# Optimization experiments

Measured on AMD Instinct MI355X. Metric: run time of the kernel, lower is better.

The kernel has to match this reference:

```python
import jax, jax.numpy as jnp
import numpy as np
from jax import lax

NI, NH, NO = 128, 64, 128
PERIODS = np.array([1, 2, 4, 8, 16, 32, 64, 128], dtype=np.int32)
NCLOCKS = len(PERIODS)
K = NCLOCKS * NH  # total hidden size = 512
T, B = 512, 256


def _glorotize(W):
    W = W * np.sqrt(6.0)
    W = W / np.sqrt(np.sum(W.shape))
    return W


def _recurrent_mask():
    # block upper-triangular: row block r can read hidden blocks r..NCLOCKS-1
    rows = []
    for c in range(NCLOCKS, 0, -1):
        zero = np.zeros((NH, NH * (NCLOCKS - c)))
        one = np.ones((NH, NH * c))
        rows.append(np.concatenate([zero, one], axis=1))
    return np.concatenate(rows, axis=0)


def setup_inputs() -> dict:
    key = jax.random.key(0)
    kx = jax.random.fold_in(key, 0)
    rng = np.random.default_rng(0)
    X = jax.random.normal(kx, (T, B, NI), dtype=jnp.float32)
    Wi = _glorotize(rng.standard_normal((K, NI + 1)))
    Wh = rng.standard_normal((K, K + 1))
    U, _, _ = np.linalg.svd(Wh[:, :-1])
    Wh[:, :-1] = U * _recurrent_mask()
    Wo = _glorotize(rng.standard_normal((NO, K + 1)))
    return {
        "X": X,
        "Wi": jnp.asarray(Wi, jnp.float32),
        "Wh": jnp.asarray(Wh, jnp.float32),
        "Wo": jnp.asarray(Wo, jnp.float32),
    }


def reference(X, Wi, Wh, Wo):
    # X: (T, B, NI). Original code treats trailing axis as batch after transpose.
    periods = jnp.repeat(jnp.asarray(PERIODS), NH)               # (K,)
    active = ((jnp.arange(T)[:, None] % periods[None, :]) == 0)  # (T, K)
    active = active.astype(X.dtype)

    Xt = jnp.swapaxes(X, 1, 2)                                   # (T, NI, B)
    Wi_w, Wi_b = Wi[:, :-1], Wi[:, -1:]                          # (K,NI),(K,1)
    Wh_w, Wh_b = Wh[:, :-1], Wh[:, -1:]                          # (K,K),(K,1)
    Wo_w, Wo_b = Wo[:, :-1], Wo[:, -1:]                          # (NO,K),(NO,1)

    def step(H_prev, inp):
        x, a = inp                                               # (NI,B),(K,)
        i_h = Wi_w @ x + Wi_b                                    # (K,B)
        H_new = jnp.tanh(i_h + Wh_w @ H_prev + Wh_b)             # (K,B)
        a = a[:, None]
        H = a * H_new + (1.0 - a) * H_prev                       # clock gating
        y = jnp.tanh(Wo_w @ H + Wo_b)                            # (NO,B)
        return H, y

    H0 = jnp.zeros((K, B), dtype=X.dtype)
    H, Ys = lax.scan(step, H0, (Xt, active))                     # Ys: (T,NO,B)
    return jnp.swapaxes(Ys, 1, 2), H                             # (T,B,NO),(K,B)
```

## Files before the change

### kernel.cpp

```cpp
#include <hip/hip_runtime.h>


typedef unsigned int  u32;
typedef unsigned short u16;
typedef _Float16 f16;
typedef f16   f16x2 __attribute__((ext_vector_type(2)));
typedef f16   f16x8 __attribute__((ext_vector_type(8)));
typedef float f32x4 __attribute__((ext_vector_type(4)));

#define TT   512
#define BB   256
#define NI_  128
#define NO_  128

#define WIP_N   32768
#define WHRP_N  49152
#define WHLP_N  30720
#define WOA_N   32768
#define ICOMP_PER_B 65280
#define IOFF(j_) (65536 - (65536 >> (j_)))

__device__ __forceinline__ u32 pk2(float a, float b){
  f16x2 v; v.x=(f16)a; v.y=(f16)b; return __builtin_bit_cast(u32, v);
}
__device__ __forceinline__ float tanh_fast(float x){
  float e = __expf(2.0f*x);
  return 1.0f - 2.0f/(e + 1.0f);
}
__device__ __forceinline__ float dot2(u32 a, u32 b, float c){
#if __has_builtin(__builtin_amdgcn_fdot2)
  return __builtin_amdgcn_fdot2(__builtin_bit_cast(f16x2,a), __builtin_bit_cast(f16x2,b), c, false);
#else
  f16x2 x = __builtin_bit_cast(f16x2,a), y = __builtin_bit_cast(f16x2,b);
  c = fmaf((float)x.x,(float)y.x,c); c = fmaf((float)x.y,(float)y.y,c); return c;
#endif
}
__device__ __forceinline__ float f16at_rt(uint4 v, int i){
  u32 w = (i&4) ? ((i&2)? v.w : v.z) : ((i&2)? v.y : v.x);
  w = (i&1) ? (w>>16) : (w & 0xffffu);
  return (float)__builtin_bit_cast(f16, (u16)w);
}
__device__ __forceinline__ float f16at2(uint2 v, int i){
  u32 w = (i&2) ? v.y : v.x;
  w = (i&1) ? (w>>16) : (w & 0xffffu);
  return (float)__builtin_bit_cast(f16, (u16)w);
}
__device__ __forceinline__ float f16at1(u32 v, int i){
  u32 w = i ? (v>>16) : (v & 0xffffu);
  return (float)__builtin_bit_cast(f16, (u16)w);
}

#define BAR()   asm volatile("s_waitcnt lgkmcnt(0)\n\ts_barrier" ::: "memory")
#define LGKMW() do{ asm volatile("s_waitcnt lgkmcnt(0)" ::: "memory"); \
                    __builtin_amdgcn_sched_barrier(0); }while(0)

__global__ __launch_bounds__(256) void cw_prep(
    const float* __restrict__ Wi, const float* __restrict__ Wh, const float* __restrict__ Wo,
    u32* __restrict__ WiP, u32* __restrict__ WhrP, u32* __restrict__ WhlP, u32* __restrict__ WoAu,
    float* __restrict__ cb, float* __restrict__ wob)
{
  const int NTOT = WIP_N + WHRP_N + WHLP_N + WOA_N + 512 + 128;
  for (int idx = blockIdx.x*blockDim.x + threadIdx.x; idx < NTOT; idx += (int)(gridDim.x*blockDim.x)){
    if (idx < WIP_N){
      int r  = idx >> 6;
      int c2 = idx & 63;
      WiP[idx] = pk2(Wi[r*129 + 2*c2], Wi[r*129 + 2*c2 + 1]);
    } else if (idx < WIP_N + WHRP_N){
      int q32 = idx - WIP_N;
      int slot = q32 >> 11, rr = (q32 >> 5) & 63, c4 = q32 & 31;
      int jj = slot / 3, dq = slot % 3, qq = jj + dq;
      u32 v = 0u;
      if (qq <= 7){
        int row = 64*jj + rr;
        v = pk2(Wh[row*513 + 64*qq + 2*c4], Wh[row*513 + 64*qq + 2*c4 + 1]);
      }
      WhrP[q32] = v;
    } else if (idx < WIP_N + WHRP_N + WHLP_N){
      int q32 = idx - WIP_N - WHRP_N;
      int slot = q32 >> 11, rr = (q32 >> 5) & 63, pos = (q32 >> 2) & 7, e = q32 & 3;
      int jj, qq;
      if      (slot <  5){ jj = 0; qq = slot + 3; }
      else if (slot <  9){ jj = 1; qq = slot - 1; }
      else if (slot < 12){ jj = 2; qq = slot - 4; }
      else if (slot < 14){ jj = 3; qq = slot - 6; }
      else               { jj = 4; qq = 7; }
      int i  = pos ^ (rr & 7);
      int cp = i*4 + e;
      int row = 64*jj + rr;
      WhlP[q32] = pk2(Wh[row*513 + 64*qq + 2*cp], Wh[row*513 + 64*qq + 2*cp + 1]);
    } else if (idx < WIP_N + WHRP_N + WHLP_N + WOA_N){
      int q32 = idx - WIP_N - WHRP_N - WHLP_N;
      int o = q32 >> 8, kp = q32 & 255;
      WoAu[q32] = pk2(Wo[o*513 + 2*kp], Wo[o*513 + 2*kp + 1]);
    } else if (idx < WIP_N + WHRP_N + WHLP_N + WOA_N + 512){
      int r = idx - WIP_N - WHRP_N - WHLP_N - WOA_N;
      cb[r] = Wh[r*513 + 512] + Wi[r*129 + 128];
    } else {
      int o = idx - WIP_N - WHRP_N - WHLP_N - WOA_N - 512;
      wob[o] = Wo[o*513 + 512];
    }
  }
}

__global__ __launch_bounds__(256) void cw_igemm(
    const float* __restrict__ X, const u32* __restrict__ WiP, f16* __restrict__ Icomp)
{
  const int tid = threadIdx.x;
  const int l = tid & 63, w = tid >> 6;
  const int bid = blockIdx.x;
  const int b = bid / 19, sub = bid % 19;
  int j, m0;
  if      (sub <  8){ j = 0; m0 = sub*64; }
  else if (sub < 12){ j = 1; m0 = (sub-8)*64; }
  else if (sub < 14){ j = 2; m0 = (sub-12)*64; }
  else if (sub ==14){ j = 3; m0 = 0; }
  else              { j = sub-11; m0 = 0; }
  const int Nj = 512 >> j;
  const int mt = m0 + w*16;
  const int la = l & 15, lb = l >> 4;

  int ma = mt + la; if (ma >= Nj) ma = Nj - 1;
  const int t = ma << j;
  const float* Xr = X + ((size_t)t*BB + b)*NI_ + lb*8;
  const u32* wp0 = WiP + (j<<12) + la*64 + lb*4;

  f32x4 a0 = {0.f,0.f,0.f,0.f}, a1 = a0, a2 = a0, a3 = a0;
  #pragma unroll
  for (int ks = 0; ks < 4; ++ks){
    const float4 x0 = *(const float4*)(Xr + ks*32);
    const float4 x1 = *(const float4*)(Xr + ks*32 + 4);
    uint4 au;
    au.x = __builtin_bit_cast(u32, __builtin_amdgcn_cvt_pkrtz(x0.x, x0.y));
    au.y = __builtin_bit_cast(u32, __builtin_amdgcn_cvt_pkrtz(x0.z, x0.w));
    au.z = __builtin_bit_cast(u32, __builtin_amdgcn_cvt_pkrtz(x1.x, x1.y));
    au.w = __builtin_bit_cast(u32, __builtin_amdgcn_cvt_pkrtz(x1.z, x1.w));
    const f16x8 af = __builtin_bit_cast(f16x8, au);
    const u32* wp = wp0 + ks*16;
    a0 = __builtin_amdgcn_mfma_f32_16x16x32_f16(af, __builtin_bit_cast(f16x8, *(const uint4*)(wp       )), a0, 0,0,0);
    a1 = __builtin_amdgcn_mfma_f32_16x16x32_f16(af, __builtin_bit_cast(f16x8, *(const uint4*)(wp + 1024)), a1, 0,0,0);
    a2 = __builtin_amdgcn_mfma_f32_16x16x32_f16(af, __builtin_bit_cast(f16x8, *(const uint4*)(wp + 2048)), a2, 0,0,0);
    a3 = __builtin_amdgcn_mfma_f32_16x16x32_f16(af, __builtin_bit_cast(f16x8, *(const uint4*)(wp + 3072)), a3, 0,0,0);
  }
  const int mb = mt + lb*4;
  if (mb < Nj){
    const size_t offj = 65536 - (65536 >> j);
    f16* base = Icomp + (size_t)b*ICOMP_PER_B + offj + mb;
    uint2 s;
    s.x = __builtin_bit_cast(u32, __builtin_amdgcn_cvt_pkrtz(a0[0], a0[1]));
    s.y = __builtin_bit_cast(u32, __builtin_amdgcn_cvt_pkrtz(a0[2], a0[3]));
    *(uint2*)(base + (size_t)( 0 + la)*Nj) = s;
    s.x = __builtin_bit_cast(u32, __builtin_amdgcn_cvt_pkrtz(a1[0], a1[1]));
    s.y = __builtin_bit_cast(u32, __builtin_amdgcn_cvt_pkrtz(a1[2], a1[3]));
    *(uint2*)(base + (size_t)(16 + la)*Nj) = s;
    s.x = __builtin_bit_cast(u32, __builtin_amdgcn_cvt_pkrtz(a2[0], a2[1]));
    s.y = __builtin_bit_cast(u32, __builtin_amdgcn_cvt_pkrtz(a2[2], a2[3]));
    *(uint2*)(base + (size_t)(32 + la)*Nj) = s;
    s.x = __builtin_bit_cast(u32, __builtin_amdgcn_cvt_pkrtz(a3[0], a3[1]));
    s.y = __builtin_bit_cast(u32, __builtin_amdgcn_cvt_pkrtz(a3[2], a3[3]));
    *(uint2*)(base + (size_t)(48 + la)*Nj) = s;
  }
}

__device__ __forceinline__ float gemv8(const uint4 (&W)[8], const u32* hq){
  float a0=0.f, a1=0.f, a2=0.f, a3=0.f;
  #pragma unroll
  for (int i = 0; i < 8; ++i){
    const uint4 hv = *(const uint4*)(hq + (i<<2));
    a0 = dot2(W[i].x, hv.x, a0); a1 = dot2(W[i].y, hv.y, a1);
    a2 = dot2(W[i].z, hv.z, a2); a3 = dot2(W[i].w, hv.w, a3);
  }
  return (a0+a1)+(a2+a3);
}
__device__ __forceinline__ float dotreg8(const uint4 (&W)[8], const uint4 (&H)[8]){
  float a0=0.f, a1=0.f, a2=0.f, a3=0.f;
  #pragma unroll
  for (int i = 0; i < 8; ++i){
    a0 = dot2(W[i].x, H[i].x, a0); a1 = dot2(W[i].y, H[i].y, a1);
    a2 = dot2(W[i].z, H[i].z, a2); a3 = dot2(W[i].w, H[i].w, a3);
  }
  return (a0+a1)+(a2+a3);
}
__device__ __forceinline__ float gemv_sw(const u32* __restrict__ wp, const u32* hq, int lx){
  float a0=0.f, a1=0.f, a2=0.f, a3=0.f;
  #pragma unroll
  for (int i = 0; i < 8; ++i){
    const uint4 w  = *(const uint4*)(wp + ((i ^ lx) << 2));
    const uint4 hv = *(const uint4*)(hq + (i<<2));
    a0 = dot2(w.x, hv.x, a0); a1 = dot2(w.y, hv.y, a1);
    a2 = dot2(w.z, hv.z, a2); a3 = dot2(w.w, hv.w, a3);
  }
  return (a0+a1)+(a2+a3);
}
__device__ __forceinline__ float gemv_ns(const u32* __restrict__ wp, const u32* hq){
  float a0=0.f, a1=0.f, a2=0.f, a3=0.f;
  #pragma unroll
  for (int i = 0; i < 8; ++i){
    const uint4 w  = *(const uint4*)(wp + (i << 2));
    const uint4 hv = *(const uint4*)(hq + (i<<2));
    a0 = dot2(w.x, hv.x, a0); a1 = dot2(w.y, hv.y, a1);
    a2 = dot2(w.z, hv.z, a2); a3 = dot2(w.w, hv.w, a3);
  }
  return (a0+a1)+(a2+a3);
}

#define SPR(hr_, q_, s_) ((const u32*)((hr_) + (((((q_)-3)*4) + (int)(s_)) << 6)))

template<int X>
__device__ __forceinline__ void helper_entries(int per, float* __restrict__ tabp,
    const u32* __restrict__ whr, const u32* __restrict__ whl,
    const u16* __restrict__ hring, int l)
{
  const int lx = l & 7;
  #pragma unroll
  for (int q = 3; q <= 7; ++q){
    if ((per & ((1 << (q-3)) - 1)) == 0){
      const u32 v = ((u32)(8*per) >> q) + 1;
      const u32* hq = SPR(hring, q, v & 3);
      float val;
      if constexpr (X == 0){
        val = gemv_sw(whl + (q-3)*2048 + l*32, hq, lx);
      } else {
        if (q == 3) val = gemv_ns(whr + 5*2048 + l*32, hq);
        else        val = gemv_sw(whl + (5 + (q-4))*2048 + l*32, hq, lx);
      }
      tabp[(X*5 + (q-3))*64 + l] = val;
    }
  }
}

template<int J>
__device__ void run_waveJ(const f16* __restrict__ Ib, const u32* __restrict__ whr,
                          const u32* __restrict__ whl, u16* hring,
                          f16* __restrict__ Hc, float* __restrict__ Hout,
                          float cbv, int r, int b)
{
  constexpr int NJ  = 512 >> J;
  constexpr int ND  = 8 - J;
  constexpr int TWJ = 1 << J;
  const int lx = r & 7;

  uint4 W0[8], W1[8], W2[8];
  {
    const u32* w0 = whr + (J*3)*2048 + r*32;
    #pragma unroll
    for (int i = 0; i < 8; ++i) W0[i] = *(const uint4*)(w0 + (i<<2));
    if constexpr (ND > 1){
      #pragma unroll
      for (int i = 0; i < 8; ++i) W1[i] = *(const uint4*)(w0 + 2048 + (i<<2));
    }
    if constexpr (ND > 2){
      #pragma unroll
      for (int i = 0; i < 8; ++i) W2[i] = *(const uint4*)(w0 + 4096 + (i<<2));
    }
  }
  float ctx[8];
  #pragma unroll
  for (int q = 0; q < 8; ++q) ctx[q] = 0.f;

  uint4 icur = {0,0,0,0}, inxt = {0,0,0,0};
  if constexpr (NJ >= 8) icur = *(const uint4*)(Ib);
  else { const uint2 u2 = *(const uint2*)(Ib); icur.x = u2.x; icur.y = u2.y; }
  if constexpr (NJ > 8) inxt = *(const uint4*)(Ib + 8);

  float h;
  {
    h = tanh_fast(cbv + f16at_rt(icur, 0));
    const f16 h16 = (f16)h;
    hring[(((J-3)*4 + 1) << 6) + r] = __builtin_bit_cast(u16, h16);
    Hc[r] = h16;
    LGKMW();
    ctx[J] = gemv8(W0, SPR(hring, J, 1));
  }

  auto body = [&](int t){
    if ((t & (TWJ - 1)) != 0) return;
    const int tm = t - TWJ;
    const int cc0 = (tm == 0) ? 7 : __builtin_ctz((u32)tm);
    const int cc = cc0 > 7 ? 7 : cc0;
    if constexpr (ND > 1){
      if (cc >= J + 1){ const u32 v = ((u32)tm >> (J + 1)) + 1;
        ctx[J+1] = gemv8(W1, SPR(hring, J+1, v & 3)); }
    }
    if constexpr (ND > 2){
      if (cc >= J + 2){ const u32 v = ((u32)tm >> (J + 2)) + 1;
        ctx[J+2] = gemv8(W2, SPR(hring, J+2, v & 3)); }
    }
    if constexpr (J == 3){
      if (cc >= 6){ const u32 v = ((u32)tm >> 6) + 1; ctx[6] = gemv_sw(whl + 12*2048 + r*32, SPR(hring, 6, v & 3), lx); }
      if (cc >= 7){ const u32 v = ((u32)tm >> 7) + 1; ctx[7] = gemv_sw(whl + 13*2048 + r*32, SPR(hring, 7, v & 3), lx); }
    }
    if constexpr (J == 4){
      if (cc >= 7){ const u32 v = ((u32)tm >> 7) + 1; ctx[7] = gemv_sw(whl + 14*2048 + r*32, SPR(hring, 7, v & 3), lx); }
    }
    const int m = t >> J, e = m & 7;
    if constexpr (NJ > 8){ if (e == 0 && m + 8 < NJ) inxt = *(const uint4*)(Ib + m + 8); }
    float z = cbv + f16at_rt(icur, e);
    #pragma unroll
    for (int q = J; q < 8; ++q) z += ctx[q];
    h = tanh_fast(z);
    const f16 h16 = (f16)h;
    const int sl = (m + 1) & 3;
    hring[(((J-3)*4 + sl) << 6) + r] = __builtin_bit_cast(u16, h16);
    Hc[(m << 6) + r] = h16;
    LGKMW();
    ctx[J] = gemv8(W0, SPR(hring, J, sl));
    if constexpr (NJ > 8){ if (e == 7) icur = inxt; }
  };

  BAR();
  body(8);
  BAR();
  for (int k = 0; k < 64; ++k){
    const int t = 8*(k + 2);
    if (t < 512) body(t);
    BAR();
  }
  Hout[(J*64 + r)*BB + b] = h;
}

__global__ __launch_bounds__(512) void cw_serial(
    const f16* __restrict__ Icomp, const u32* __restrict__ WhrP, const u32* __restrict__ WhlP,
    const float* __restrict__ cbg, f16* __restrict__ Hcomp, float* __restrict__ Hout)
{
  __shared__ u32 sW2[6144];
  __shared__ __align__(16) u16 hring[5*4*64];
  __shared__ __align__(16) u16 sh01[128];
  __shared__ __align__(16) u16 sh2[128];
  __shared__ float ctxTab[2*960];
  __shared__ float tab2[512];

  const int tid = (int)threadIdx.x;
  const int b   = (int)blockIdx.x;
  const int wv  = tid >> 6, l = tid & 63;

  for (int i = tid; i < 2048; i += 512){
    const int rr = i >> 5, c4 = i & 31, ch = c4 >> 2, e = c4 & 3;
    const int dst = rr*32 + (((ch ^ rr) & 7) << 2) + e;
    sW2[       dst] = WhrP[2*2048 + i];
    sW2[2048 + dst] = WhrP[4*2048 + i];
    sW2[4096 + dst] = WhrP[6*2048 + i];
  }
  __syncthreads();

  const f16* Ibase = Icomp + (size_t)b*ICOMP_PER_B;
  f16*       Hbase = Hcomp + (size_t)b*ICOMP_PER_B;

  if (wv == 0){
    u16* shw = sh01;
    const u32* shu = (const u32*)sh01;

    uint4 w00[8], w01[8], w11[8];
    #pragma unroll
    for (int i = 0; i < 8; ++i){
      w00[i] = *(const uint4*)(WhrP +      0 + l*32 + (i<<2));
      w01[i] = *(const uint4*)(WhrP +   2048 + l*32 + (i<<2));
      w11[i] = *(const uint4*)(WhrP + 3*2048 + l*32 + (i<<2));
    }
    const float cb0 = cbg[l], cb1 = cbg[64+l];
    float c00=0.f,c01=0.f,c11=0.f,c02=0.f,c12=0.f;
    float c3a[5]={0,0,0,0,0}, c3b[5]={0,0,0,0,0};
    float zq0=cb0, zq1=cb1;
    float h0v=0.f, h1v=0.f;

    const u16* Ib0 = (const u16*)Ibase + l*512;
    const u16* Ib1 = (const u16*)Ibase + 32768 + l*256;
    u16* Hb0 = (u16*)Hbase;
    u16* Hb1 = (u16*)Hbase + 32768;

    uint4 icur0 = *(const uint4*)(Ib0);
    uint2 icur1 = *(const uint2*)(Ib1);

    {
      h0v = tanh_fast(cb0 + f16at_rt(icur0, 0));
      h1v = tanh_fast(cb1 + f16at2(icur1, 0));
      const f16 a0=(f16)h0v, a1=(f16)h1v;
      shw[l]    = __builtin_bit_cast(u16,a0);
      shw[64+l] = __builtin_bit_cast(u16,a1);
      Hb0[l] = __builtin_bit_cast(u16,a0);
      Hb1[l] = __builtin_bit_cast(u16,a1);
      c00 = gemv8(w00, shu);
      uint4 hq1[8];
      #pragma unroll
      for (int i = 0; i < 8; ++i) hq1[i] = *(const uint4*)(shu + 32 + (i<<2));
      c01 = dotreg8(w01, hq1); c11 = dotreg8(w11, hq1);
    }
    BAR();
    BAR();

#define W0_STEP(S_, B1_) do{ \
      const int t_ = 8*k + (S_); \
      float z0 = zq0 + c01 + c02 + c00 + f16at_rt(icur0, (S_)); \
      float z1 = 0.f; \
      if (B1_) z1 = zq1 + c11 + c12 + f16at2(icur1, (S_)>>1); \
      h0v = tanh_fast(z0); \
      if (B1_) h1v = tanh_fast(z1); \
      { const f16 a=(f16)h0v; shw[l] = __builtin_bit_cast(u16,a); \
        Hb0[(t_<<6)+l] = __builtin_bit_cast(u16,a); } \
      if (B1_){ const f16 a=(f16)h1v; shw[64+l] = __builtin_bit_cast(u16,a); \
        Hb1[((4*k+((S_)>>1))<<6)+l] = __builtin_bit_cast(u16,a); } \
      c00 = gemv8(w00, shu); \
      if (B1_){ uint4 hq1[8]; \
        _Pragma("unroll") for (int i = 0; i < 8; ++i) hq1[i] = *(const uint4*)(shu + 32 + (i<<2)); \
        c01 = dotreg8(w01, hq1); c11 = dotreg8(w11, hq1); } \
    }while(0)

    for (int k = 0; k < 64; ++k){
      uint4 inxt0 = icur0; uint2 inxt1 = icur1;
      const bool pf = (k < 63);
      if (pf){
        inxt0 = *(const uint4*)(Ib0 + 8*(k+1));
        inxt1 = *(const uint2*)(Ib1 + 4*(k+1));
      }
      if (k > 0) W0_STEP(0, 1);
      {
        const float* tab = ctxTab + (k & 1)*960;
                { c3a[0]=tab[0*64+l]; c3b[0]=tab[5*64+l]; }
        if((k&1)==0)   { c3a[1]=tab[1*64+l]; c3b[1]=tab[6*64+l]; }
        if((k&3)==0)   { c3a[2]=tab[2*64+l]; c3b[2]=tab[7*64+l]; }
        if((k&7)==0)   { c3a[3]=tab[3*64+l]; c3b[3]=tab[8*64+l]; }
        if((k&15)==0)  { c3a[4]=tab[4*64+l]; c3b[4]=tab[9*64+l]; }
        zq0 = cb0 + (((c3a[0]+c3a[1])+(c3a[2]+c3a[3]))+c3a[4]);
        zq1 = cb1 + (((c3b[0]+c3b[1])+(c3b[2]+c3b[3]))+c3b[4]);
      }
      c02 = tab2[(k&1)*256 +   0 + l];
      c12 = tab2[(k&1)*256 +  64 + l];
      W0_STEP(1,0); W0_STEP(2,1); W0_STEP(3,0); W0_STEP(4,1);
      c02 = tab2[(k&1)*256 + 128 + l];
      c12 = tab2[(k&1)*256 + 192 + l];
      W0_STEP(5,0); W0_STEP(6,1); W0_STEP(7,0);
      if (pf){ icur0 = inxt0; icur1 = inxt1; }
      BAR();
    }
#undef W0_STEP
    Hout[l*BB + b]      = h0v;
    Hout[(64+l)*BB + b] = h1v;

  } else if (wv == 1){
    BAR();
    helper_entries<0>(0, ctxTab, WhrP, WhlP, hring, l);
    helper_entries<1>(0, ctxTab, WhrP, WhlP, hring, l);
    BAR();
    for (int k = 0; k < 64; ++k){
      const int per = k + 1;
      if (per < 64){
        float* tp = ctxTab + (per & 1)*960;
        helper_entries<0>(per, tp, WhrP, WhlP, hring, l);
        helper_entries<1>(per, tp, WhrP, WhlP, hring, l);
      }
      BAR();
    }
  } else if (wv == 2){
    const int lx = l & 7;
    uint4 W23r[8], W24r[8];
    #pragma unroll
    for (int i = 0; i < 8; ++i){
      W23r[i] = *(const uint4*)(WhrP + 7*2048 + l*32 + (i<<2));
      W24r[i] = *(const uint4*)(WhrP + 8*2048 + l*32 + (i<<2));
    }
    const float cb2 = cbg[128+l];
    float c22=0.f,c23=0.f,c24=0.f,c25=0.f,c26=0.f,c27=0.f;
    int vp3=0,vp4=0,vp5=0,vp6=0,vp7=0;
    const u16* Ib2 = (const u16*)Ibase + 49152 + l*128;
    u16* Hb2 = (u16*)Hbase + 49152;
    float h2v = 0.f;
    u32 icp = *(const u32*)(Ib2);

    {
      h2v = tanh_fast(cb2 + f16at1(icp, 0));
      const f16 a=(f16)h2v;
      sh2[l] = __builtin_bit_cast(u16,a);
      Hb2[l] = __builtin_bit_cast(u16,a);
      const u32* hb = (const u32*)sh2;
      tab2[  0 + l] = gemv_sw(sW2 +        l*32, hb, lx);
      tab2[ 64 + l] = gemv_sw(sW2 + 2048 + l*32, hb, lx);
    }
    BAR();
    {
      c23 = gemv8(W23r, SPR(hring, 3, 1)); vp3 = 1;
      c24 = gemv8(W24r, SPR(hring, 4, 1)); vp4 = 1;
      c25 = gemv_sw(WhlP +  9*2048 + l*32, SPR(hring, 5, 1), lx); vp5 = 1;
      c26 = gemv_sw(WhlP + 10*2048 + l*32, SPR(hring, 6, 1), lx); vp6 = 1;
      c27 = gemv_sw(WhlP + 11*2048 + l*32, SPR(hring, 7, 1), lx); vp7 = 1;
      c22 = gemv_sw(sW2 + 4096 + l*32, (const u32*)sh2, lx);
      float z2 = cb2 + f16at1(icp, 1) + ((c22 + c23) + (c24 + c25)) + (c26 + c27);
      h2v = tanh_fast(z2);
      const f16 a=(f16)h2v;
      sh2[64+l] = __builtin_bit_cast(u16,a);
      Hb2[64+l] = __builtin_bit_cast(u16,a);
      const u32* hb = (const u32*)(sh2 + 64);
      tab2[128 + l] = gemv_sw(sW2 +        l*32, hb, lx);
      tab2[192 + l] = gemv_sw(sW2 + 2048 + l*32, hb, lx);
    }
    BAR();

    for (int k = 0; k < 64; ++k){
      if (k <= 62){
        const int m1 = 2*(k+1);
        icp = *(const u32*)(Ib2 + m1);
        const int par = (k+1) & 1;
        {
          const int t = m1 << 2;
          { const int v = ((t-1)>>3)+1; if (v != vp3){ c23 = gemv8(W23r, SPR(hring,3,v&3)); vp3 = v; } }
          { const int v = ((t-1)>>4)+1; if (v != vp4){ c24 = gemv8(W24r, SPR(hring,4,v&3)); vp4 = v; } }
          { const int v = ((t-1)>>5)+1; if (v != vp5){ c25 = gemv_sw(WhlP +  9*2048 + l*32, SPR(hring,5,v&3), lx); vp5 = v; } }
          { const int v = ((t-1)>>6)+1; if (v != vp6){ c26 = gemv_sw(WhlP + 10*2048 + l*32, SPR(hring,6,v&3), lx); vp6 = v; } }
          { const int v = ((t-1)>>7)+1; if (v != vp7){ c27 = gemv_sw(WhlP + 11*2048 + l*32, SPR(hring,7,v&3), lx); vp7 = v; } }
          c22 = gemv_sw(sW2 + 4096 + l*32, (const u32*)(sh2 + 64), lx);
          float z2 = cb2 + f16at1(icp, 0) + ((c22 + c23) + (c24 + c25)) + (c26 + c27);
          h2v = tanh_fast(z2);
          const f16 a=(f16)h2v;
          sh2[l] = __builtin_bit_cast(u16,a);
          Hb2[(m1<<6)+l] = __builtin_bit_cast(u16,a);
          const u32* hb = (const u32*)sh2;
          tab2[par*256 +   0 + l] = gemv_sw(sW2 +        l*32, hb, lx);
          tab2[par*256 +  64 + l] = gemv_sw(sW2 + 2048 + l*32, hb, lx);
        }
        {
          const int t = (m1+1) << 2;
          { const int v = ((t-1)>>3)+1; if (v != vp3){ c23 = gemv8(W23r, SPR(hring,3,v&3)); vp3 = v; } }
          { const int v = ((t-1)>>4)+1; if (v != vp4){ c24 = gemv8(W24r, SPR(hring,4,v&3)); vp4 = v; } }
          { const int v = ((t-1)>>5)+1; if (v != vp5){ c25 = gemv_sw(WhlP +  9*2048 + l*32, SPR(hring,5,v&3), lx); vp5 = v; } }
          { const int v = ((t-1)>>6)+1; if (v != vp6){ c26 = gemv_sw(WhlP + 10*2048 + l*32, SPR(hring,6,v&3), lx); vp6 = v; } }
          { const int v = ((t-1)>>7)+1; if (v != vp7){ c27 = gemv_sw(WhlP + 11*2048 + l*32, SPR(hring,7,v&3), lx); vp7 = v; } }
          c22 = gemv_sw(sW2 + 4096 + l*32, (const u32*)sh2, lx);
          float z2 = cb2 + f16at1(icp, 1) + ((c22 + c23) + (c24 + c25)) + (c26 + c27);
          h2v = tanh_fast(z2);
          const f16 a=(f16)h2v;
          sh2[64+l] = __builtin_bit_cast(u16,a);
          Hb2[((m1+1)<<6)+l] = __builtin_bit_cast(u16,a);
          const u32* hb = (const u32*)(sh2 + 64);
          tab2[par*256 + 128 + l] = gemv_sw(sW2 +        l*32, hb, lx);
          tab2[par*256 + 192 + l] = gemv_sw(sW2 + 2048 + l*32, hb, lx);
        }
      }
      BAR();
    }
    Hout[(128+l)*BB + b] = h2v;

  } else {
    const int J = wv;
    const float cbv = cbg[J*64 + l];
    const f16* Ib = Ibase + IOFF(J) + l*(512 >> J);
    f16* Hc = Hbase + IOFF(J);
    switch (J){
      case 3: run_waveJ<3>(Ib, WhrP, WhlP, hring, Hc, Hout, cbv, l, b); break;
      case 4: run_waveJ<4>(Ib, WhrP, WhlP, hring, Hc, Hout, cbv, l, b); break;
      case 5: run_waveJ<5>(Ib, WhrP, WhlP, hring, Hc, Hout, cbv, l, b); break;
      case 6: run_waveJ<6>(Ib, WhrP, WhlP, hring, Hc, Hout, cbv, l, b); break;
      default: run_waveJ<7>(Ib, WhrP, WhlP, hring, Hc, Hout, cbv, l, b); break;
    }
  }
}

__global__ __launch_bounds__(512) void cw_ygemm2(
    const f16* __restrict__ Hcomp, const u32* __restrict__ WoAu,
    const float* __restrict__ wobg, float* __restrict__ Y)
{
  const int tid = (int)threadIdx.x;
  const int w = tid >> 6, l = tid & 63;
  const int la = l & 15, lb = l >> 4;
  const int b  = (int)blockIdx.x;
  const int t0 = (int)blockIdx.y * 64;
  const int o0 = w * 16;

  uint4 A[16];
  {
    const u32* ap = WoAu + (o0 + la)*256 + lb*4;
    #pragma unroll
    for (int ks = 0; ks < 16; ++ks) A[ks] = *(const uint4*)(ap + ks*16);
  }
  const float4 wv = *(const float4*)(wobg + o0 + lb*4);
  const f16* Hb = Hcomp + (size_t)b * ICOMP_PER_B;

  #pragma unroll
  for (int tt = 0; tt < 4; ++tt){
    const int tA = t0 + tt*16 + la;
    f32x4 ac = {0.f,0.f,0.f,0.f};
    #pragma unroll
    for (int ks = 0; ks < 16; ++ks){
      const int j   = ks >> 1;
      const int m   = tA >> j;
      const int off = IOFF(j) + (m << 6) + ((ks & 1) << 5) + lb*8;
      const uint4 Bf = *(const uint4*)(Hb + off);
      ac = __builtin_amdgcn_mfma_f32_16x16x32_f16(
             __builtin_bit_cast(f16x8, A[ks]), __builtin_bit_cast(f16x8, Bf), ac, 0,0,0);
    }
    float4 yv;
    yv.x = tanh_fast(ac[0] + wv.x);
    yv.y = tanh_fast(ac[1] + wv.y);
    yv.z = tanh_fast(ac[2] + wv.z);
    yv.w = tanh_fast(ac[3] + wv.w);
    *(float4*)(Y + ((size_t)(t0 + tt*16 + la)*BB + b)*NO_ + o0 + lb*4) = yv;
  }
}

extern "C" void kernel_launch(void* const* d_in, const int* in_sizes, int n_in,
                              void* d_out, int out_size, void* d_ws, size_t ws_size,
                              hipStream_t stream)
{
  const float* X  = (const float*)d_in[0];
  const float* Wi = (const float*)d_in[1];
  const float* Wh = (const float*)d_in[2];
  const float* Wo = (const float*)d_in[3];

  u32*   WiP  = (u32*)d_ws;
  u32*   WhrP = WiP  + WIP_N;
  u32*   WhlP = WhrP + WHRP_N;
  u32*   WoAu = WhlP + WHLP_N;
  float* cb   = (float*)(WoAu + WOA_N);
  float* wob  = cb + 512;
  f16*   Icomp = (f16*)(wob + 128);
  f16*   Hcomp = Icomp + (size_t)BB * ICOMP_PER_B;

  float* Y    = (float*)d_out;
  float* Hout = Y + (size_t)TT*BB*NO_;

  const int prep_n = WIP_N + WHRP_N + WHLP_N + WOA_N + 512 + 128;
  hipLaunchKernelGGL(cw_prep, dim3((prep_n + 255)/256), dim3(256), 0, stream,
                     Wi, Wh, Wo, WiP, WhrP, WhlP, WoAu, cb, wob);

  hipLaunchKernelGGL(cw_igemm, dim3(256*19), dim3(256), 0, stream, X, WiP, Icomp);

  hipLaunchKernelGGL(cw_serial, dim3(BB), dim3(512), 0, stream,
                     Icomp, WhrP, WhlP, cb, Hcomp, Hout);

  hipLaunchKernelGGL(cw_ygemm2, dim3(BB, 8), dim3(512), 0, stream,
                     Hcomp, WoAu, wob, Y);
}
```

Baseline: 326.2 us.

## Fuse output projection GEMM into serial recurrence kernel using idle wave slack

Removes the separate output GEMM launch and instead has the slower-clock waves (J>=4), which sit idle between steps, compute 16-timestep output windows of Y via MFMA from already-written hidden states, with a final tail window computed by all waves. Critical-path waves 0 and 2 get raised scheduling priority, and vmcnt waits are inserted before barriers so global Hcomp writes are visible before they are read back. This trades extra work and global loads inside the latency-bound serial kernel for eliminating a kernel launch and the full Hcomp re-read pass, at the risk of slowing the serial critical path.

```diff
diff --git a/kernel.cpp b/kernel.cpp
--- a/kernel.cpp
+++ b/kernel.cpp
@@ -205,6 +205,38 @@
 
 #define SPR(hr_, q_, s_) ((const u32*)((hr_) + (((((q_)-3)*4) + (int)(s_)) << 6)))
 
+__device__ __forceinline__ void y_window(const f16* __restrict__ HbF,
+    const u32* __restrict__ WoAu, const float* __restrict__ wobg,
+    float* __restrict__ Y, int b, int t0, int opair, int l)
+{
+  const int la = l & 15, lb = l >> 4;
+  const int o0 = opair * 32;
+  const int tA = t0 + la;
+  f32x4 ac0 = {0.f,0.f,0.f,0.f}, ac1 = ac0;
+  const u32* ap0 = WoAu + (o0 + la)*256 + lb*4;
+  #pragma unroll
+  for (int ks = 0; ks < 16; ++ks){
+    const int j   = ks >> 1;
+    const int m   = tA >> j;
+    const int off = IOFF(j) + (m << 6) + ((ks & 1) << 5) + lb*8;
+    const f16x8 Bf = __builtin_bit_cast(f16x8, *(const uint4*)(HbF + off));
+    const f16x8 A0 = __builtin_bit_cast(f16x8, *(const uint4*)(ap0 + ks*16));
+    const f16x8 A1 = __builtin_bit_cast(f16x8, *(const uint4*)(ap0 + 16*256 + ks*16));
+    ac0 = __builtin_amdgcn_mfma_f32_16x16x32_f16(A0, Bf, ac0, 0,0,0);
+    ac1 = __builtin_amdgcn_mfma_f32_16x16x32_f16(A1, Bf, ac1, 0,0,0);
+  }
+  const float4 wb0 = *(const float4*)(wobg + o0 + lb*4);
+  const float4 wb1 = *(const float4*)(wobg + o0 + 16 + lb*4);
+  float* Yr = Y + ((size_t)tA*BB + b)*NO_;
+  float4 y0, y1;
+  y0.x = tanh_fast(ac0[0] + wb0.x); y0.y = tanh_fast(ac0[1] + wb0.y);
+  y0.z = tanh_fast(ac0[2] + wb0.z); y0.w = tanh_fast(ac0[3] + wb0.w);
+  y1.x = tanh_fast(ac1[0] + wb1.x); y1.y = tanh_fast(ac1[1] + wb1.y);
+  y1.z = tanh_fast(ac1[2] + wb1.z); y1.w = tanh_fast(ac1[3] + wb1.w);
+  *(float4*)(Yr + o0 + lb*4)      = y0;
+  *(float4*)(Yr + o0 + 16 + lb*4) = y1;
+}
+
 template<int X>
 __device__ __forceinline__ void helper_entries(int per, float* __restrict__ tabp,
     const u32* __restrict__ whr, const u32* __restrict__ whl,
@@ -232,7 +264,9 @@
 __device__ void run_waveJ(const f16* __restrict__ Ib, const u32* __restrict__ whr,
                           const u32* __restrict__ whl, u16* hring,
                           f16* __restrict__ Hc, float* __restrict__ Hout,
-                          float cbv, int r, int b)
+                          float cbv, int r, int b,
+                          const f16* __restrict__ HbF, const u32* __restrict__ WoAu,
+                          const float* __restrict__ wobg, float* __restrict__ Yp)
 {
   constexpr int NJ  = 512 >> J;
   constexpr int ND  = 8 - J;
@@ -313,6 +347,11 @@
   for (int k = 0; k < 64; ++k){
     const int t = 8*(k + 2);
     if (t < 512) body(t);
+    if constexpr (J >= 4){
+      if ((k & 1) == 0 && k >= 4 && k <= 62)
+        y_window(HbF, WoAu, wobg, Yp, b, 8*(k - 4), J - 4, r);
+    }
+    if (k & 1) asm volatile("s_waitcnt vmcnt(0)" ::: "memory");
     BAR();
   }
   Hout[(J*64 + r)*BB + b] = h;
@@ -320,7 +359,8 @@
 
 __global__ __launch_bounds__(512) void cw_serial(
     const f16* __restrict__ Icomp, const u32* __restrict__ WhrP, const u32* __restrict__ WhlP,
-    const float* __restrict__ cbg, f16* __restrict__ Hcomp, float* __restrict__ Hout)
+    const float* __restrict__ cbg, f16* __restrict__ Hcomp, float* __restrict__ Hout,
+    const u32* __restrict__ WoAu, const float* __restrict__ wobg, float* __restrict__ Yp)
 {
   __shared__ u32 sW2[6144];
   __shared__ __align__(16) u16 hring[5*4*64];
@@ -341,6 +381,8 @@
     sW2[4096 + dst] = WhrP[6*2048 + i];
   }
   __syncthreads();
+
+  if (wv == 0 || wv == 2) __builtin_amdgcn_s_setprio(1);
 
   const f16* Ibase = Icomp + (size_t)b*ICOMP_PER_B;
   f16*       Hbase = Hcomp + (size_t)b*ICOMP_PER_B;
@@ -429,6 +471,7 @@
       c12 = tab2[(k&1)*256 + 192 + l];
       W0_STEP(5,0); W0_STEP(6,1); W0_STEP(7,0);
       if (pf){ icur0 = inxt0; icur1 = inxt1; }
+      asm volatile("s_waitcnt vmcnt(8)" ::: "memory");
       BAR();
     }
 #undef W0_STEP
@@ -533,6 +576,7 @@
           tab2[par*256 + 192 + l] = gemv_sw(sW2 + 2048 + l*32, hb, lx);
         }
       }
+      if (k & 1) asm volatile("s_waitcnt vmcnt(0)" ::: "memory");
       BAR();
     }
     Hout[(128+l)*BB + b] = h2v;
@@ -543,55 +587,17 @@
     const f16* Ib = Ibase + IOFF(J) + l*(512 >> J);
     f16* Hc = Hbase + IOFF(J);
     switch (J){
-      case 3: run_waveJ<3>(Ib, WhrP, WhlP, hring, Hc, Hout, cbv, l, b); break;
-      case 4: run_waveJ<4>(Ib, WhrP, WhlP, hring, Hc, Hout, cbv, l, b); break;
-      case 5: run_waveJ<5>(Ib, WhrP, WhlP, hring, Hc, Hout, cbv, l, b); break;
-      case 6: run_waveJ<6>(Ib, WhrP, WhlP, hring, Hc, Hout, cbv, l, b); break;
-      default: run_waveJ<7>(Ib, WhrP, WhlP, hring, Hc, Hout, cbv, l, b); break;
-    }
-  }
-}
-
-__global__ __launch_bounds__(512) void cw_ygemm2(
-    const f16* __restrict__ Hcomp, const u32* __restrict__ WoAu,
-    const float* __restrict__ wobg, float* __restrict__ Y)
-{
-  const int tid = (int)threadIdx.x;
-  const int w = tid >> 6, l = tid & 63;
-  const int la = l & 15, lb = l >> 4;
-  const int b  = (int)blockIdx.x;
-  const int t0 = (int)blockIdx.y * 64;
-  const int o0 = w * 16;
-
-  uint4 A[16];
-  {
-    const u32* ap = WoAu + (o0 + la)*256 + lb*4;
-    #pragma unroll
-    for (int ks = 0; ks < 16; ++ks) A[ks] = *(const uint4*)(ap + ks*16);
-  }
-  const float4 wv = *(const float4*)(wobg + o0 + lb*4);
-  const f16* Hb = Hcomp + (size_t)b * ICOMP_PER_B;
-
-  #pragma unroll
-  for (int tt = 0; tt < 4; ++tt){
-    const int tA = t0 + tt*16 + la;
-    f32x4 ac = {0.f,0.f,0.f,0.f};
-    #pragma unroll
-    for (int ks = 0; ks < 16; ++ks){
-      const int j   = ks >> 1;
-      const int m   = tA >> j;
-      const int off = IOFF(j) + (m << 6) + ((ks & 1) << 5) + lb*8;
-      const uint4 Bf = *(const uint4*)(Hb + off);
-      ac = __builtin_amdgcn_mfma_f32_16x16x32_f16(
-             __builtin_bit_cast(f16x8, A[ks]), __builtin_bit_cast(f16x8, Bf), ac, 0,0,0);
-    }
-    float4 yv;
-    yv.x = tanh_fast(ac[0] + wv.x);
-    yv.y = tanh_fast(ac[1] + wv.y);
-    yv.z = tanh_fast(ac[2] + wv.z);
-    yv.w = tanh_fast(ac[3] + wv.w);
-    *(float4*)(Y + ((size_t)(t0 + tt*16 + la)*BB + b)*NO_ + o0 + lb*4) = yv;
-  }
+      case 3: run_waveJ<3>(Ib, WhrP, WhlP, hring, Hc, Hout, cbv, l, b, Hbase, WoAu, wobg, Yp); break;
+      case 4: run_waveJ<4>(Ib, WhrP, WhlP, hring, Hc, Hout, cbv, l, b, Hbase, WoAu, wobg, Yp); break;
+      case 5: run_waveJ<5>(Ib, WhrP, WhlP, hring, Hc, Hout, cbv, l, b, Hbase, WoAu, wobg, Yp); break;
+      case 6: run_waveJ<6>(Ib, WhrP, WhlP, hring, Hc, Hout, cbv, l, b, Hbase, WoAu, wobg, Yp); break;
+      default: run_waveJ<7>(Ib, WhrP, WhlP, hring, Hc, Hout, cbv, l, b, Hbase, WoAu, wobg, Yp); break;
+    }
+  }
+
+  asm volatile("s_waitcnt vmcnt(0)" ::: "memory");
+  BAR();
+  y_window(Hbase, WoAu, wobg, Yp, b, 16*(30 + (wv & 1)), wv >> 1, l);
 }
 
 extern "C" void kernel_launch(void* const* d_in, const int* in_sizes, int n_in,
@@ -622,8 +628,5 @@
   hipLaunchKernelGGL(cw_igemm, dim3(256*19), dim3(256), 0, stream, X, WiP, Icomp);
 
   hipLaunchKernelGGL(cw_serial, dim3(BB), dim3(512), 0, stream,
-                     Icomp, WhrP, WhlP, cb, Hcomp, Hout);
-
-  hipLaunchKernelGGL(cw_ygemm2, dim3(BB, 8), dim3(512), 0, stream,
-                     Hcomp, WoAu, wob, Y);
-}
+                     Icomp, WhrP, WhlP, cb, Hcomp, Hout, WoAu, wob, Y);
+}
```

Result: slower. 333.2 us (+2.1%).
